# Performance work log

Hardware: AMD Instinct MI355X
Metric: run time of the kernel (lower is better)

Reference implementation:

```python
import jax, jax.numpy as jnp
import numpy as np

B, T, D = 32, 512, 64
P = 16          # token_t_size
OV = 8          # token_t_overlap
DM = 512        # d_model
STRIDE = P - OV
NW = (T - P) // STRIDE + 1  # 63 windows per channel


def setup_inputs() -> dict:
    key = jax.random.key(0)
    k0, k1, k2, k3, k4 = jax.random.split(key, 5)
    x = jax.random.normal(k0, (B, T, D), jnp.float32)
    Wt = jax.random.normal(k1, (DM, P), jnp.float32) / np.sqrt(P).astype(np.float32)
    bt = jax.random.normal(k2, (DM,), jnp.float32) * 0.01
    Wd = jax.random.normal(k3, (DM, D), jnp.float32) / np.sqrt(D).astype(np.float32)
    bd = jax.random.normal(k4, (DM,), jnp.float32) * 0.01
    return {"x": x, "Wt": Wt, "bt": bt, "Wd": Wd, "bd": bd}


def reference(x, Wt, bt, Wd, bd):
    # Sliding windows: starts = 0, stride, 2*stride, ...
    starts = jnp.arange(NW) * STRIDE                    # [NW]
    idx = starts[:, None] + jnp.arange(P)               # [NW, P]
    patches = x[:, idx, :]                              # [B, NW, P, D]
    # Original loop order: d outer, window inner -> token = d*NW + w
    temporal = jnp.einsum('bwpd,mp->bdwm', patches, Wt) + bt  # [B, D, NW, DM]
    temporal = temporal.reshape(B, D * NW, DM)
    # Feature tokens: per-timestep Linear(D -> DM) == one batched matmul
    feature = jnp.einsum('btd,md->btm', x, Wd) + bd     # [B, T, DM]
    return jnp.concatenate([temporal, feature], axis=1)  # [B, D*NW + T, DM]
```

## Files before the change

kernel.cpp:

```cpp
#include <hip/hip_runtime.h>
#include <cstddef>
#include <cstdint>

namespace {

constexpr int kB = 32, kT = 512, kD = 64, kP = 16, kNW = 63, kDM = 512;
constexpr int kRows = kD * kNW + kT;
constexpr int kPS = 132;
constexpr int kNBF = kB * (kT / 16);
constexpr int kNBT = kB * kD;

typedef float f32x4  __attribute__((ext_vector_type(4)));
typedef short bf16x8 __attribute__((ext_vector_type(8)));

constexpr int kWdOff = 32768;

__device__ __forceinline__ unsigned short bf16_rne(float f) {
    unsigned int u = __float_as_uint(f);
    u += 0x7fffu + ((u >> 16) & 1u);
    return (unsigned short)(u >> 16);
}
__device__ __forceinline__ float bf16_f(unsigned short h) {
    return __uint_as_float(((unsigned int)h) << 16);
}

__global__ __launch_bounds__(256)
void prep_k(const float* __restrict__ Wt, const float* __restrict__ Wd,
            unsigned short* __restrict__ ws)
{
    const int gid = blockIdx.x * 256 + threadIdx.x;
    for (int e = gid; e < 32 * 64; e += gridDim.x * 256) {
        const int n = e >> 6, l = e & 63;
        unsigned short* dh = ws + ((size_t)(n * 2 + 0) * 64 + l) * 8;
        unsigned short* dl = ws + ((size_t)(n * 2 + 1) * 64 + l) * 8;
        if (l < 32) {
            const int row = 16 * n + (l & 15);
            const int p0  = 8 * (l >> 4);
            #pragma unroll
            for (int j = 0; j < 8; ++j) {
                float f = Wt[row * kP + p0 + j];
                unsigned short h = bf16_rne(f);
                dh[j] = h;
                dl[j] = bf16_rne(f - bf16_f(h));
            }
        } else {
            #pragma unroll
            for (int j = 0; j < 8; ++j) { dh[j] = 0; dl[j] = 0; }
        }
    }
    for (int e = gid; e < 32 * 2 * 64; e += gridDim.x * 256) {
        const int n = e >> 7, kc = (e >> 6) & 1, l = e & 63;
        const int row = 16 * n + (l & 15);
        const int d0  = 32 * kc + 8 * (l >> 4);
        unsigned short* dh = ws + kWdOff + ((size_t)((n * 2 + kc) * 2 + 0) * 64 + l) * 8;
        unsigned short* dl = ws + kWdOff + ((size_t)((n * 2 + kc) * 2 + 1) * 64 + l) * 8;
        #pragma unroll
        for (int j = 0; j < 8; ++j) {
            float f = Wd[row * kD + d0 + j];
            unsigned short h = bf16_rne(f);
            dh[j] = h;
            dl[j] = bf16_rne(f - bf16_f(h));
        }
    }
}

__global__ __launch_bounds__(256)
void main_k(const float* __restrict__ x, const unsigned short* __restrict__ ws,
            const float* __restrict__ bt, const float* __restrict__ bd,
            float* __restrict__ out)
{
    __shared__ __align__(16) float slab[4 * 16 * kPS];
    __shared__ __align__(16) unsigned short hi_s[640];
    __shared__ __align__(16) unsigned short lo_s[640];
    const int tid = threadIdx.x, lane = tid & 63, wave = tid >> 6;
    float* myslab = slab + wave * 16 * kPS;

    const int swrow = lane >> 5;
    const int swcol = 4 * (lane & 31);
    const int wrbase = (lane & 15) * kPS + 4 * (lane >> 4);

    if ((int)blockIdx.x >= kNBF) {
        const int blk = blockIdx.x - kNBF;
        const int b = blk >> 6, d = blk & (kD - 1);

        #pragma unroll
        for (int i = 0; i < 2; ++i) {
            const int t = tid + 256 * i;
            const float f = x[(b * kT + t) * kD + d];
            const unsigned short h = bf16_rne(f);
            hi_s[t] = h;
            lo_s[t] = bf16_rne(f - bf16_f(h));
        }
        if (tid < 128) { hi_s[512 + tid] = 0; lo_s[512 + tid] = 0; }
        __syncthreads();

        bf16x8 Ah[8], Al[8];
        #pragma unroll
        for (int i = 0; i < 8; ++i) {
            const int n = 8 * wave + i;
            Ah[i] = *(const bf16x8*)(ws + ((n * 2 + 0) * 64 + lane) * 8);
            Al[i] = *(const bf16x8*)(ws + ((n * 2 + 1) * 64 + lane) * 8);
        }

        const f32x4 biasv = *(const f32x4*)(bt + 128 * wave + swcol);

        float* orow = out + (size_t)b * kRows * kDM + (size_t)(d * kNW) * kDM + 128 * wave;

        for (int g = 0; g < 4; ++g) {
            const int toff = 128 * g + 8 * (lane & 15) + 8 * (lane >> 4);
            const bf16x8 Bh = *(const bf16x8*)(hi_s + toff);
            const bf16x8 Bl = *(const bf16x8*)(lo_s + toff);

            #pragma unroll
            for (int i = 0; i < 8; ++i) {
                f32x4 acc = {0.f, 0.f, 0.f, 0.f};
                acc = __builtin_amdgcn_mfma_f32_16x16x32_bf16(Ah[i], Bh, acc, 0, 0, 0);
                acc = __builtin_amdgcn_mfma_f32_16x16x32_bf16(Al[i], Bh, acc, 0, 0, 0);
                acc = __builtin_amdgcn_mfma_f32_16x16x32_bf16(Ah[i], Bl, acc, 0, 0, 0);
                *(f32x4*)(myslab + wrbase + 16 * i) = acc;
            }
            #pragma unroll
            for (int k = 0; k < 8; ++k) {
                const int r    = 2 * k + swrow;
                const int wrow = 16 * g + r;
                const f32x4 v = *(const f32x4*)(myslab + r * kPS + swcol);
                if (wrow < kNW)
                    *(f32x4*)(orow + (size_t)wrow * kDM + swcol) = v + biasv;
            }
        }
    } else {
        const int blk = blockIdx.x;
        const int b = blk >> 5, tc = blk & 31;
        const int t  = tc * 16 + (lane & 15);
        const int d0 = 8 * (lane >> 4);

        const float* xrow = x + ((size_t)b * kT + t) * kD;
        bf16x8 Bh[2], Bl[2];
        #pragma unroll
        for (int kc = 0; kc < 2; ++kc) {
            #pragma unroll
            for (int j = 0; j < 8; ++j) {
                const float f = xrow[32 * kc + d0 + j];
                const unsigned short h = bf16_rne(f);
                Bh[kc][j] = (short)h;
                Bl[kc][j] = (short)bf16_rne(f - bf16_f(h));
            }
        }

        const f32x4 biasv = *(const f32x4*)(bd + 128 * wave + swcol);
        const unsigned short* wsd = ws + kWdOff;

        #pragma unroll
        for (int i = 0; i < 8; ++i) {
            const int n = 8 * wave + i;
            const bf16x8 Ah0 = *(const bf16x8*)(wsd + (((n * 2 + 0) * 2 + 0) * 64 + lane) * 8);
            const bf16x8 Al0 = *(const bf16x8*)(wsd + (((n * 2 + 0) * 2 + 1) * 64 + lane) * 8);
            const bf16x8 Ah1 = *(const bf16x8*)(wsd + (((n * 2 + 1) * 2 + 0) * 64 + lane) * 8);
            const bf16x8 Al1 = *(const bf16x8*)(wsd + (((n * 2 + 1) * 2 + 1) * 64 + lane) * 8);
            f32x4 acc = {0.f, 0.f, 0.f, 0.f};
            acc = __builtin_amdgcn_mfma_f32_16x16x32_bf16(Ah0, Bh[0], acc, 0, 0, 0);
            acc = __builtin_amdgcn_mfma_f32_16x16x32_bf16(Al0, Bh[0], acc, 0, 0, 0);
            acc = __builtin_amdgcn_mfma_f32_16x16x32_bf16(Ah0, Bl[0], acc, 0, 0, 0);
            acc = __builtin_amdgcn_mfma_f32_16x16x32_bf16(Ah1, Bh[1], acc, 0, 0, 0);
            acc = __builtin_amdgcn_mfma_f32_16x16x32_bf16(Al1, Bh[1], acc, 0, 0, 0);
            acc = __builtin_amdgcn_mfma_f32_16x16x32_bf16(Ah1, Bl[1], acc, 0, 0, 0);
            *(f32x4*)(myslab + wrbase + 16 * i) = acc;
        }

        float* orows = out + (size_t)b * kRows * kDM
                     + (size_t)(kD * kNW + tc * 16) * kDM + 128 * wave;
        #pragma unroll
        for (int k = 0; k < 8; ++k) {
            const int r = 2 * k + swrow;
            const f32x4 v = *(const f32x4*)(myslab + r * kPS + swcol);
            *(f32x4*)(orows + (size_t)r * kDM + swcol) = v + biasv;
        }
    }
}

}

extern "C" void kernel_launch(void* const* d_in, const int* in_sizes, int n_in,
                              void* d_out, int out_size, void* d_ws, size_t ws_size,
                              hipStream_t stream) {
    const float* x  = (const float*)d_in[0];
    const float* Wt = (const float*)d_in[1];
    const float* bt = (const float*)d_in[2];
    const float* Wd = (const float*)d_in[3];
    const float* bd = (const float*)d_in[4];
    float* out = (float*)d_out;
    unsigned short* ws = (unsigned short*)d_ws;

    hipLaunchKernelGGL(prep_k, dim3(16),          dim3(256), 0, stream, Wt, Wd, ws);
    hipLaunchKernelGGL(main_k, dim3(kNBF + kNBT), dim3(256), 0, stream, x, ws, bt, bd, out);
}
```

Before: 64.55 us.

## Fuse weight bf16 split into main kernel and drop prep launch

Removes the separate prep kernel that pre-split Wt and Wd into bf16 hi/lo fragments in workspace. Each block now loads fp32 weights directly with vector loads and performs the hi/lo split in registers, saving a launch and the workspace round trip. The temporal blocks are reordered to come first in the grid, and x loads in the feature path are vectorised. The cost is redundant conversion arithmetic repeated in every block.

```diff
diff --git a/kernel.cpp b/kernel.cpp
--- a/kernel.cpp
+++ b/kernel.cpp
@@ -7,13 +7,11 @@
 constexpr int kB = 32, kT = 512, kD = 64, kP = 16, kNW = 63, kDM = 512;
 constexpr int kRows = kD * kNW + kT;
 constexpr int kPS = 132;
+constexpr int kNBT = kB * kD;
 constexpr int kNBF = kB * (kT / 16);
-constexpr int kNBT = kB * kD;
 
 typedef float f32x4  __attribute__((ext_vector_type(4)));
 typedef short bf16x8 __attribute__((ext_vector_type(8)));
-
-constexpr int kWdOff = 32768;
 
 __device__ __forceinline__ unsigned short bf16_rne(float f) {
     unsigned int u = __float_as_uint(f);
@@ -24,49 +22,19 @@
     return __uint_as_float(((unsigned int)h) << 16);
 }
 
-__global__ __launch_bounds__(256)
-void prep_k(const float* __restrict__ Wt, const float* __restrict__ Wd,
-            unsigned short* __restrict__ ws)
-{
-    const int gid = blockIdx.x * 256 + threadIdx.x;
-    for (int e = gid; e < 32 * 64; e += gridDim.x * 256) {
-        const int n = e >> 6, l = e & 63;
-        unsigned short* dh = ws + ((size_t)(n * 2 + 0) * 64 + l) * 8;
-        unsigned short* dl = ws + ((size_t)(n * 2 + 1) * 64 + l) * 8;
-        if (l < 32) {
-            const int row = 16 * n + (l & 15);
-            const int p0  = 8 * (l >> 4);
-            #pragma unroll
-            for (int j = 0; j < 8; ++j) {
-                float f = Wt[row * kP + p0 + j];
-                unsigned short h = bf16_rne(f);
-                dh[j] = h;
-                dl[j] = bf16_rne(f - bf16_f(h));
-            }
-        } else {
-            #pragma unroll
-            for (int j = 0; j < 8; ++j) { dh[j] = 0; dl[j] = 0; }
-        }
-    }
-    for (int e = gid; e < 32 * 2 * 64; e += gridDim.x * 256) {
-        const int n = e >> 7, kc = (e >> 6) & 1, l = e & 63;
-        const int row = 16 * n + (l & 15);
-        const int d0  = 32 * kc + 8 * (l >> 4);
-        unsigned short* dh = ws + kWdOff + ((size_t)((n * 2 + kc) * 2 + 0) * 64 + l) * 8;
-        unsigned short* dl = ws + kWdOff + ((size_t)((n * 2 + kc) * 2 + 1) * 64 + l) * 8;
-        #pragma unroll
-        for (int j = 0; j < 8; ++j) {
-            float f = Wd[row * kD + d0 + j];
-            unsigned short h = bf16_rne(f);
-            dh[j] = h;
-            dl[j] = bf16_rne(f - bf16_f(h));
-        }
+__device__ __forceinline__ void split8(const float* v, bf16x8& hi, bf16x8& lo) {
+    #pragma unroll
+    for (int j = 0; j < 8; ++j) {
+        const unsigned short h = bf16_rne(v[j]);
+        hi[j] = (short)h;
+        lo[j] = (short)bf16_rne(v[j] - bf16_f(h));
     }
 }
 
 __global__ __launch_bounds__(256)
-void main_k(const float* __restrict__ x, const unsigned short* __restrict__ ws,
-            const float* __restrict__ bt, const float* __restrict__ bd,
+void main_k(const float* __restrict__ x,
+            const float* __restrict__ Wt, const float* __restrict__ bt,
+            const float* __restrict__ Wd, const float* __restrict__ bd,
             float* __restrict__ out)
 {
     __shared__ __align__(16) float slab[4 * 16 * kPS];
@@ -79,8 +47,8 @@
     const int swcol = 4 * (lane & 31);
     const int wrbase = (lane & 15) * kPS + 4 * (lane >> 4);
 
-    if ((int)blockIdx.x >= kNBF) {
-        const int blk = blockIdx.x - kNBF;
+    if ((int)blockIdx.x < kNBT) {
+        const int blk = blockIdx.x;
         const int b = blk >> 6, d = blk & (kD - 1);
 
         #pragma unroll
@@ -95,15 +63,27 @@
         __syncthreads();
 
         bf16x8 Ah[8], Al[8];
-        #pragma unroll
-        for (int i = 0; i < 8; ++i) {
-            const int n = 8 * wave + i;
-            Ah[i] = *(const bf16x8*)(ws + ((n * 2 + 0) * 64 + lane) * 8);
-            Al[i] = *(const bf16x8*)(ws + ((n * 2 + 1) * 64 + lane) * 8);
+        {
+            const int row = (lane & 15);
+            const int p0  = 8 * (lane >> 4);
+            #pragma unroll
+            for (int i = 0; i < 8; ++i) {
+                const int n = 8 * wave + i;
+                float v[8];
+                if (lane < 32) {
+                    const f32x4* wp = (const f32x4*)(Wt + (16 * n + row) * kP + p0);
+                    const f32x4 a = wp[0], c = wp[1];
+                    v[0]=a.x; v[1]=a.y; v[2]=a.z; v[3]=a.w;
+                    v[4]=c.x; v[5]=c.y; v[6]=c.z; v[7]=c.w;
+                } else {
+                    #pragma unroll
+                    for (int j = 0; j < 8; ++j) v[j] = 0.f;
+                }
+                split8(v, Ah[i], Al[i]);
+            }
         }
 
         const f32x4 biasv = *(const f32x4*)(bt + 128 * wave + swcol);
-
         float* orow = out + (size_t)b * kRows * kDM + (size_t)(d * kNW) * kDM + 128 * wave;
 
         for (int g = 0; g < 4; ++g) {
@@ -129,7 +109,7 @@
             }
         }
     } else {
-        const int blk = blockIdx.x;
+        const int blk = blockIdx.x - kNBT;
         const int b = blk >> 5, tc = blk & 31;
         const int t  = tc * 16 + (lane & 15);
         const int d0 = 8 * (lane >> 4);
@@ -138,25 +118,35 @@
         bf16x8 Bh[2], Bl[2];
         #pragma unroll
         for (int kc = 0; kc < 2; ++kc) {
-            #pragma unroll
-            for (int j = 0; j < 8; ++j) {
-                const float f = xrow[32 * kc + d0 + j];
-                const unsigned short h = bf16_rne(f);
-                Bh[kc][j] = (short)h;
-                Bl[kc][j] = (short)bf16_rne(f - bf16_f(h));
-            }
+            float v[8];
+            const f32x4* xp = (const f32x4*)(xrow + 32 * kc + d0);
+            const f32x4 a = xp[0], c = xp[1];
+            v[0]=a.x; v[1]=a.y; v[2]=a.z; v[3]=a.w;
+            v[4]=c.x; v[5]=c.y; v[6]=c.z; v[7]=c.w;
+            split8(v, Bh[kc], Bl[kc]);
         }
 
         const f32x4 biasv = *(const f32x4*)(bd + 128 * wave + swcol);
-        const unsigned short* wsd = ws + kWdOff;
+        const int row = (lane & 15);
 
         #pragma unroll
         for (int i = 0; i < 8; ++i) {
             const int n = 8 * wave + i;
-            const bf16x8 Ah0 = *(const bf16x8*)(wsd + (((n * 2 + 0) * 2 + 0) * 64 + lane) * 8);
-            const bf16x8 Al0 = *(const bf16x8*)(wsd + (((n * 2 + 0) * 2 + 1) * 64 + lane) * 8);
-            const bf16x8 Ah1 = *(const bf16x8*)(wsd + (((n * 2 + 1) * 2 + 0) * 64 + lane) * 8);
-            const bf16x8 Al1 = *(const bf16x8*)(wsd + (((n * 2 + 1) * 2 + 1) * 64 + lane) * 8);
+            bf16x8 Ah0, Al0, Ah1, Al1;
+            {
+                const float* wrow = Wd + (size_t)(16 * n + row) * kD;
+                float v[8];
+                const f32x4* wp0 = (const f32x4*)(wrow + d0);
+                f32x4 a = wp0[0], c = wp0[1];
+                v[0]=a.x; v[1]=a.y; v[2]=a.z; v[3]=a.w;
+                v[4]=c.x; v[5]=c.y; v[6]=c.z; v[7]=c.w;
+                split8(v, Ah0, Al0);
+                const f32x4* wp1 = (const f32x4*)(wrow + 32 + d0);
+                a = wp1[0]; c = wp1[1];
+                v[0]=a.x; v[1]=a.y; v[2]=a.z; v[3]=a.w;
+                v[4]=c.x; v[5]=c.y; v[6]=c.z; v[7]=c.w;
+                split8(v, Ah1, Al1);
+            }
             f32x4 acc = {0.f, 0.f, 0.f, 0.f};
             acc = __builtin_amdgcn_mfma_f32_16x16x32_bf16(Ah0, Bh[0], acc, 0, 0, 0);
             acc = __builtin_amdgcn_mfma_f32_16x16x32_bf16(Al0, Bh[0], acc, 0, 0, 0);
@@ -189,8 +179,7 @@
     const float* Wd = (const float*)d_in[3];
     const float* bd = (const float*)d_in[4];
     float* out = (float*)d_out;
-    unsigned short* ws = (unsigned short*)d_ws;
 
-    hipLaunchKernelGGL(prep_k, dim3(16),          dim3(256), 0, stream, Wt, Wd, ws);
-    hipLaunchKernelGGL(main_k, dim3(kNBF + kNBT), dim3(256), 0, stream, x, ws, bt, bd, out);
+    hipLaunchKernelGGL(main_k, dim3(kNBT + kNBF), dim3(256), 0, stream,
+                       x, Wt, bt, Wd, bd, out);
 }
```

New measurement: 67.09 us. +3.9%, slower.
